# Performance work log

Hardware: AMD Instinct MI355X
Metric: run time of the kernel (lower is better)

The kernel has to match this reference:

```python
import jax, jax.numpy as jnp
import numpy as np

B, T, H = 2048, 2048, 32  # batch, sequence steps (columns of input), hidden size


def setup_inputs() -> dict:
    key = jax.random.key(0)
    ks = jax.random.split(key, 5)
    stdv = 1.0 / np.sqrt(H)
    u = lambda k, shp: jax.random.uniform(k, shp, jnp.float32, -stdv, stdv)
    return {
        "x": jax.random.normal(ks[0], (B, T), jnp.float32),
        "weight_ih": u(ks[1], (4 * H, 1)),
        "weight_hh": u(ks[2], (4 * H, H)),
        "bias_ih": u(ks[3], (4 * H,)),
        "bias_hh": u(ks[4], (4 * H,)),
    }


def reference(x, weight_ih, weight_hh, bias_ih, bias_hh):
    Bn, Tn = x.shape
    Hn = weight_hh.shape[1]
    xs = x.T[:, :, None]              # (T, B, 1): step-major inputs
    bias = bias_ih + bias_hh          # (4H,)

    def step(carry, x_t):
        h, c = carry                  # (B, H) each
        gates = x_t @ weight_ih.T + h @ weight_hh.T + bias  # (B, 4H)
        i, f, g, o = jnp.split(gates, 4, axis=1)
        i = jax.nn.sigmoid(i)
        f = jax.nn.sigmoid(f)
        g = jnp.tanh(g)
        o = jax.nn.sigmoid(o)
        # row 0 of the original skips the forget term entirely; with c0 = 0,
        # f * c0 == 0, so this is identical math.
        c_new = f * c + i * g
        h_new = o * jnp.tanh(c_new)
        return (h_new, c_new), h_new

    h0 = jnp.zeros((Bn, Hn), x.dtype)
    c0 = jnp.zeros((Bn, Hn), x.dtype)
    _, ys = jax.lax.scan(step, (h0, c0), xs)   # ys: (T, B, H)
    # torch.cat(h_matrix, 1): step-major blocks of width H along dim 1
    return jnp.transpose(ys, (1, 0, 2)).reshape(Bn, Tn * Hn)
```

## Files before the change

### kernel.cpp

```cpp
#include <hip/hip_runtime.h>
#include <hip/hip_bf16.h>
#include <hip/hip_fp16.h>


#define Bsz 2048
#define Tsz 2048
#define Hsz 32

typedef _Float16 v2h __attribute__((ext_vector_type(2)));

__device__ __forceinline__ float fast_rcp(float x) { return __builtin_amdgcn_rcpf(x); }
__device__ __forceinline__ float fast_exp2(float x) { return __builtin_amdgcn_exp2f(x); }
__device__ __forceinline__ float fast_tanh(float x) {
    return __fmaf_rn(2.0f, fast_rcp(1.0f + fast_exp2(-2.885390082f * x)), -1.0f);
}

__device__ __forceinline__ float fdot2(v2h a, v2h b, float c) {
#if __has_builtin(__builtin_amdgcn_fdot2)
    return __builtin_amdgcn_fdot2(a, b, c, false);
#else
    return __fmaf_rn((float)a.x, (float)b.x, __fmaf_rn((float)a.y, (float)b.y, c));
#endif
}

__device__ __forceinline__ void plswap(float a, float b, float& r0, float& r1) {
#if __has_builtin(__builtin_amdgcn_permlane32_swap)
    auto r = __builtin_amdgcn_permlane32_swap(__float_as_uint(a), __float_as_uint(b),
                                              false, false);
    r0 = __uint_as_float(r[0]);
    r1 = __uint_as_float(r[1]);
#else
    const bool hi = (threadIdx.x & 32) != 0;
    r0 = hi ? __shfl_xor(b, 32) : a;
    r1 = hi ? b : __shfl_xor(a, 32);
#endif
}

__global__ __launch_bounds__(256, 2) void lstm_fwd_kernel(
    const float* __restrict__ x,
    const float* __restrict__ w_ih,
    const float* __restrict__ w_hh,
    const float* __restrict__ b_ih,
    const float* __restrict__ b_hh,
    float* __restrict__ out)
{
    __shared__ _Float16 hbuf[4][32];

    const int lane = threadIdx.x & 63;
    const int k    = lane & 31;
    const int hf   = lane >> 5;
    const int wv   = threadIdx.x >> 6;
    const int b    = blockIdx.x * 4 + wv;

    v2h W[4][8];
#pragma unroll
    for (int g = 0; g < 4; ++g) {
        const float4* wr =
            reinterpret_cast<const float4*>(w_hh + (size_t)(g * 32 + k) * 32 + hf * 16);
#pragma unroll
        for (int q = 0; q < 4; ++q) {
            float4 v = wr[q];
            W[g][2 * q]     = (v2h){(_Float16)v.x, (_Float16)v.y};
            W[g][2 * q + 1] = (v2h){(_Float16)v.z, (_Float16)v.w};
        }
    }
    const int gA = hf ? 2 : 0, gB = gA + 1;
    const float wiA = w_ih[gA * 32 + k], bsA = b_ih[gA * 32 + k] + b_hh[gA * 32 + k];
    const float wiB = w_ih[gB * 32 + k], bsB = b_ih[gB * 32 + k] + b_hh[gB * 32 + k];

    const float B1 = hf ? -2.885390082f : -1.442695041f;
    const float A1 = hf ? 2.0f : 1.0f;
    const float C1 = hf ? -1.0f : 0.0f;

    float c = 0.0f, h = 0.0f, hprev = 0.0f;
    hbuf[wv][k] = (_Float16)0.0f;

    const float4* xq = reinterpret_cast<const float4*>(x + (size_t)b * Tsz);
    float* op = out + (size_t)b * (size_t)(Tsz * Hsz) + hf * 32 + k;

    union Uq { uint4 q; v2h h2[4]; };

    auto steps8 = [&](float4 xA, float4 xB) {
        const float xts[8] = {xA.x, xA.y, xA.z, xA.w, xB.x, xB.y, xB.z, xB.w};
#pragma unroll
        for (int tt = 0; tt < 8; ++tt) {
            Uq u0 = *reinterpret_cast<const Uq*>(&hbuf[wv][hf * 16]);
            Uq u1 = *reinterpret_cast<const Uq*>(&hbuf[wv][hf * 16 + 8]);
            const float xt = xts[tt];

            float s0 = 0.0f, s1 = 0.0f, s2 = 0.0f, s3 = 0.0f;
#pragma unroll
            for (int j = 0; j < 4; ++j) {
                s0 = fdot2(W[0][j], u0.h2[j], s0);
                s1 = fdot2(W[1][j], u0.h2[j], s1);
                s2 = fdot2(W[2][j], u0.h2[j], s2);
                s3 = fdot2(W[3][j], u0.h2[j], s3);
            }
#pragma unroll
            for (int j = 0; j < 4; ++j) {
                s0 = fdot2(W[0][4 + j], u1.h2[j], s0);
                s1 = fdot2(W[1][4 + j], u1.h2[j], s1);
                s2 = fdot2(W[2][4 + j], u1.h2[j], s2);
                s3 = fdot2(W[3][4 + j], u1.h2[j], s3);
            }

            float r0, r1;
            plswap(s0, s2, r0, r1);
            const float v1 = r0 + r1 + __fmaf_rn(wiA, xt, bsA);
            plswap(s1, s3, r0, r1);
            const float v2 = r0 + r1 + __fmaf_rn(wiB, xt, bsB);

            const float a1 = __fmaf_rn(A1, fast_rcp(1.0f + fast_exp2(B1 * v1)), C1);
            const float a2 = fast_rcp(1.0f + fast_exp2(-1.442695041f * v2));

            float i_, g_, f_, o_;
            plswap(a1, a1, i_, g_);
            plswap(a2, a2, f_, o_);

            c = __fmaf_rn(f_, c, i_ * g_);
            h = o_ * fast_tanh(c);

            hbuf[wv][k] = (_Float16)h;

            if (tt & 1) {
                *op = hf ? h : hprev;
                op += 64;
            } else {
                hprev = h;
            }
        }
    };

    float4 xc0 = xq[0], xc1 = xq[1];
    const int last_base = (Tsz >> 2) - 2;
#pragma unroll 1
    for (int t0 = 0; t0 < Tsz; t0 += 16) {
        const int i1 = (t0 >> 2) + 2;
        float4 xn0 = xq[i1], xn1 = xq[i1 + 1];
        steps8(xc0, xc1);
        const int i2 = ((t0 >> 2) + 4 > last_base) ? last_base : (t0 >> 2) + 4;
        float4 xm0 = xq[i2], xm1 = xq[i2 + 1];
        steps8(xn0, xn1);
        xc0 = xm0; xc1 = xm1;
    }
}

extern "C" void kernel_launch(void* const* d_in, const int* in_sizes, int n_in,
                              void* d_out, int out_size, void* d_ws, size_t ws_size,
                              hipStream_t stream) {
    const float* x    = (const float*)d_in[0];
    const float* w_ih = (const float*)d_in[1];
    const float* w_hh = (const float*)d_in[2];
    const float* b_ih = (const float*)d_in[3];
    const float* b_hh = (const float*)d_in[4];
    float* out = (float*)d_out;

    dim3 grid(Bsz / 4);
    dim3 block(256);
    lstm_fwd_kernel<<<grid, block, 0, stream>>>(x, w_ih, w_hh, b_ih, b_hh, out);
}
```

Measured before the change: 610.2 us.

## Split gates across half-waves with full-K dot products and LDS-staged x tiles

Each half-wave now computes two whole gate rows over all 32 hidden inputs, reading the full h vector from LDS. The old scheme split K between the half-waves and combined partial sums with cross-lane swaps, so this removes two permlane swaps and the adds from the serial step chain. Each lane now holds 32 packed weight registers and does 32 fdot2 per step instead of 32 split across four accumulators, with four LDS reads of h instead of two. The per-row x input is now double-buffered through LDS in 64-step tiles with a register prefetch, replacing the float4 global loads.

```diff
diff --git a/kernel.cpp b/kernel.cpp
--- a/kernel.cpp
+++ b/kernel.cpp
@@ -1,5 +1,4 @@
 #include <hip/hip_runtime.h>
-#include <hip/hip_bf16.h>
 #include <hip/hip_fp16.h>
 
 
@@ -11,15 +10,15 @@
 
 __device__ __forceinline__ float fast_rcp(float x) { return __builtin_amdgcn_rcpf(x); }
 __device__ __forceinline__ float fast_exp2(float x) { return __builtin_amdgcn_exp2f(x); }
-__device__ __forceinline__ float fast_tanh(float x) {
-    return __fmaf_rn(2.0f, fast_rcp(1.0f + fast_exp2(-2.885390082f * x)), -1.0f);
-}
 
-__device__ __forceinline__ float fdot2(v2h a, v2h b, float c) {
+__device__ __forceinline__ float fdot2(uint a, uint b, float c) {
 #if __has_builtin(__builtin_amdgcn_fdot2)
-    return __builtin_amdgcn_fdot2(a, b, c, false);
+    return __builtin_amdgcn_fdot2(__builtin_bit_cast(v2h, a),
+                                  __builtin_bit_cast(v2h, b), c, false);
 #else
-    return __fmaf_rn((float)a.x, (float)b.x, __fmaf_rn((float)a.y, (float)b.y, c));
+    v2h av = __builtin_bit_cast(v2h, a), bv = __builtin_bit_cast(v2h, b);
+    return __fmaf_rn((float)av.x, (float)bv.x,
+                     __fmaf_rn((float)av.y, (float)bv.y, c));
 #endif
 }
 
@@ -45,103 +44,99 @@
     float* __restrict__ out)
 {
     __shared__ _Float16 hbuf[4][32];
+    __shared__ float    xtile[4][2][64];
 
     const int lane = threadIdx.x & 63;
     const int k    = lane & 31;
-    const int hf   = lane >> 5;
+    const int gp   = lane >> 5;
     const int wv   = threadIdx.x >> 6;
     const int b    = blockIdx.x * 4 + wv;
 
-    v2h W[4][8];
+    uint WA[16], WB[16];
+    {
+        const float* rA = w_hh + (size_t)(gp * 64 + k) * 32;
+        const float* rB = rA + 32 * 32;
 #pragma unroll
-    for (int g = 0; g < 4; ++g) {
-        const float4* wr =
-            reinterpret_cast<const float4*>(w_hh + (size_t)(g * 32 + k) * 32 + hf * 16);
-#pragma unroll
-        for (int q = 0; q < 4; ++q) {
-            float4 v = wr[q];
-            W[g][2 * q]     = (v2h){(_Float16)v.x, (_Float16)v.y};
-            W[g][2 * q + 1] = (v2h){(_Float16)v.z, (_Float16)v.w};
+        for (int j = 0; j < 16; ++j) {
+            WA[j] = __builtin_bit_cast(
+                uint, (v2h){(_Float16)rA[2 * j], (_Float16)rA[2 * j + 1]});
+            WB[j] = __builtin_bit_cast(
+                uint, (v2h){(_Float16)rB[2 * j], (_Float16)rB[2 * j + 1]});
         }
     }
-    const int gA = hf ? 2 : 0, gB = gA + 1;
-    const float wiA = w_ih[gA * 32 + k], bsA = b_ih[gA * 32 + k] + b_hh[gA * 32 + k];
-    const float wiB = w_ih[gB * 32 + k], bsB = b_ih[gB * 32 + k] + b_hh[gB * 32 + k];
+    const int jA = gp * 64 + k, jB = jA + 32;
+    const float wiA = w_ih[jA], bsA = b_ih[jA] + b_hh[jA];
+    const float wiB = w_ih[jB], bsB = b_ih[jB] + b_hh[jB];
 
-    const float B1 = hf ? -2.885390082f : -1.442695041f;
-    const float A1 = hf ? 2.0f : 1.0f;
-    const float C1 = hf ? -1.0f : 0.0f;
+    const float B1 = gp ? -2.885390082f : -1.442695041f;
+    const float A1 = gp ? 2.0f : 1.0f;
+    const float C1 = gp ? -1.0f : 0.0f;
 
     float c = 0.0f, h = 0.0f, hprev = 0.0f;
     hbuf[wv][k] = (_Float16)0.0f;
 
-    const float4* xq = reinterpret_cast<const float4*>(x + (size_t)b * Tsz);
-    float* op = out + (size_t)b * (size_t)(Tsz * Hsz) + hf * 32 + k;
+    const float* xrow = x + (size_t)b * Tsz;
+    float* op = out + (size_t)b * (size_t)(Tsz * Hsz) + gp * 32 + k;
+    const uint4* hl = reinterpret_cast<const uint4*>(&hbuf[wv][0]);
 
-    union Uq { uint4 q; v2h h2[4]; };
+    xtile[wv][0][lane] = xrow[lane];
+    float xv = xrow[64 + lane];
 
-    auto steps8 = [&](float4 xA, float4 xB) {
-        const float xts[8] = {xA.x, xA.y, xA.z, xA.w, xB.x, xB.y, xB.z, xB.w};
+#pragma unroll 1
+    for (int t0 = 0; t0 < Tsz; t0 += 64) {
+        const int cur = (t0 >> 6) & 1;
+        xtile[wv][cur ^ 1][lane] = xv;
+        int pf = t0 + 128; if (pf >= Tsz) pf = Tsz - 64;
+        xv = xrow[pf + lane];
+        const float* xl = &xtile[wv][cur][0];
+
+#pragma unroll 1
+        for (int tb = 0; tb < 64; tb += 8) {
 #pragma unroll
-        for (int tt = 0; tt < 8; ++tt) {
-            Uq u0 = *reinterpret_cast<const Uq*>(&hbuf[wv][hf * 16]);
-            Uq u1 = *reinterpret_cast<const Uq*>(&hbuf[wv][hf * 16 + 8]);
-            const float xt = xts[tt];
+            for (int u = 0; u < 8; ++u) {
+                uint4 q0 = hl[0], q1 = hl[1], q2 = hl[2], q3 = hl[3];
+                const uint hh[16] = {q0.x, q0.y, q0.z, q0.w,
+                                     q1.x, q1.y, q1.z, q1.w,
+                                     q2.x, q2.y, q2.z, q2.w,
+                                     q3.x, q3.y, q3.z, q3.w};
+                const float xt = xl[tb + u];
 
-            float s0 = 0.0f, s1 = 0.0f, s2 = 0.0f, s3 = 0.0f;
+                float sA0 = 0.f, sA1 = 0.f, sB0 = 0.f, sB1 = 0.f;
 #pragma unroll
-            for (int j = 0; j < 4; ++j) {
-                s0 = fdot2(W[0][j], u0.h2[j], s0);
-                s1 = fdot2(W[1][j], u0.h2[j], s1);
-                s2 = fdot2(W[2][j], u0.h2[j], s2);
-                s3 = fdot2(W[3][j], u0.h2[j], s3);
-            }
+                for (int j = 0; j < 8; ++j) {
+                    sA0 = fdot2(WA[j], hh[j], sA0);
+                    sB0 = fdot2(WB[j], hh[j], sB0);
+                }
 #pragma unroll
-            for (int j = 0; j < 4; ++j) {
-                s0 = fdot2(W[0][4 + j], u1.h2[j], s0);
-                s1 = fdot2(W[1][4 + j], u1.h2[j], s1);
-                s2 = fdot2(W[2][4 + j], u1.h2[j], s2);
-                s3 = fdot2(W[3][4 + j], u1.h2[j], s3);
-            }
+                for (int j = 8; j < 16; ++j) {
+                    sA1 = fdot2(WA[j], hh[j], sA1);
+                    sB1 = fdot2(WB[j], hh[j], sB1);
+                }
+                const float pA = (sA0 + sA1) + __fmaf_rn(wiA, xt, bsA);
+                const float pB = (sB0 + sB1) + __fmaf_rn(wiB, xt, bsB);
 
-            float r0, r1;
-            plswap(s0, s2, r0, r1);
-            const float v1 = r0 + r1 + __fmaf_rn(wiA, xt, bsA);
-            plswap(s1, s3, r0, r1);
-            const float v2 = r0 + r1 + __fmaf_rn(wiB, xt, bsB);
+                const float a1 = __fmaf_rn(A1, fast_rcp(1.0f + fast_exp2(B1 * pA)), C1);
+                const float a2 = fast_rcp(1.0f + fast_exp2(-1.442695041f * pB));
 
-            const float a1 = __fmaf_rn(A1, fast_rcp(1.0f + fast_exp2(B1 * v1)), C1);
-            const float a2 = fast_rcp(1.0f + fast_exp2(-1.442695041f * v2));
+                float i_, g_, f_, o_;
+                plswap(a1, a1, i_, g_);
+                plswap(a2, a2, f_, o_);
 
-            float i_, g_, f_, o_;
-            plswap(a1, a1, i_, g_);
-            plswap(a2, a2, f_, o_);
+                c = __fmaf_rn(f_, c, i_ * g_);
+                const float th =
+                    __fmaf_rn(2.0f, fast_rcp(1.0f + fast_exp2(-2.885390082f * c)), -1.0f);
+                h = o_ * th;
 
-            c = __fmaf_rn(f_, c, i_ * g_);
-            h = o_ * fast_tanh(c);
+                hbuf[wv][k] = (_Float16)h;
 
-            hbuf[wv][k] = (_Float16)h;
-
-            if (tt & 1) {
-                *op = hf ? h : hprev;
-                op += 64;
-            } else {
-                hprev = h;
+                if (u & 1) {
+                    *op = gp ? h : hprev;
+                    op += 64;
+                } else {
+                    hprev = h;
+                }
             }
         }
-    };
-
-    float4 xc0 = xq[0], xc1 = xq[1];
-    const int last_base = (Tsz >> 2) - 2;
-#pragma unroll 1
-    for (int t0 = 0; t0 < Tsz; t0 += 16) {
-        const int i1 = (t0 >> 2) + 2;
-        float4 xn0 = xq[i1], xn1 = xq[i1 + 1];
-        steps8(xc0, xc1);
-        const int i2 = ((t0 >> 2) + 4 > last_base) ? last_base : (t0 >> 2) + 4;
-        float4 xm0 = xq[i2], xm1 = xq[i2 + 1];
-        steps8(xn0, xn1);
-        xc0 = xm0; xc1 = xm1;
     }
 }
 
```

Result: no change. 606.2 us (-0.6%).
